# Kernel optimization log

Measured on AMD Instinct MI355X. Metric: run time of the kernel, lower is better.

The kernel has to match this reference:

```python
import jax, jax.numpy as jnp
import numpy as np

SIGMA = 2.0
EPS = 1e-8

N, P = 4, 64
Z, Y, X = 32, 128, 128


def setup_inputs() -> dict:
    key = jax.random.key(0)
    k1, k2 = jax.random.split(key)
    logits = jax.random.normal(k1, (N, 1, Z, Y, X), dtype=jnp.float32)
    # float (z,y,x) coordinates uniformly inside the grid
    dims = jnp.array([Z, Y, X], dtype=jnp.float32)
    pts = jax.random.uniform(k2, (N, P, 3), dtype=jnp.float32) * dims
    return {"logits": logits, "pts": pts}


def reference(logits, pts):
    # logits: [N,1,Z,Y,X]; pts: [N,P,3] in (z,y,x)
    n, _, z, y, x = logits.shape
    dt = logits.dtype
    s = jax.nn.sigmoid(logits[:, 0])  # [N,Z,Y,X]

    zz = jnp.arange(z, dtype=dt)
    yy = jnp.arange(y, dtype=dt)
    xx = jnp.arange(x, dtype=dt)

    # squared distances, broadcast to [N,P,Z,Y,X] only at the sum
    dz2 = (zz[None, None, :, None, None] - pts[:, :, 0, None, None, None]) ** 2  # [N,P,Z,1,1]
    dy2 = (yy[None, None, None, :, None] - pts[:, :, 1, None, None, None]) ** 2  # [N,P,1,Y,1]
    dx2 = (xx[None, None, None, None, :] - pts[:, :, 2, None, None, None]) ** 2  # [N,P,1,1,X]

    K = jnp.exp(-(dz2 + dy2 + dx2) / (2.0 * SIGMA * SIGMA))  # [N,P,Z,Y,X]
    denom = K.sum(axis=1)  # [N,Z,Y,X]  (alpha_bg == 0)
    w = s / jnp.maximum(denom, EPS)  # [N,Z,Y,X]
    # m_p = sum_v K[p,v] * s[v] / denom[v]
    m = jnp.einsum('npzyx,nzyx->np', K, w)  # [N,P]
    point_term = -jnp.log(jnp.maximum(m, EPS)).mean(axis=1)  # [N]
    return point_term.mean()  # reduction='mean'
```

## Files before the change

### kernel.cpp

```cpp
#include <hip/hip_runtime.h>
#include <math.h>

constexpr int N_ = 4, P_ = 64, Z_ = 32, Y_ = 128, X_ = 128;
constexpr float EPSF = 1e-8f;
constexpr float INV2S2 = 0.125f;

typedef short v8s __attribute__((ext_vector_type(8)));
typedef float v4f __attribute__((ext_vector_type(4)));

__device__ __forceinline__ short bf16(float f) {
    unsigned u = __float_as_uint(f);
    u = u + 0x7fffu + ((u >> 16) & 1u);
    return (short)(u >> 16);
}

__global__ __launch_bounds__(256) void k_main(const float* __restrict__ logits,
                                              const float* __restrict__ pts,
                                              float* __restrict__ part) {
    const int b = blockIdx.x;
    const int n  = b >> 6;
    const int z  = (b >> 1) & 31;
    const int y0 = (b & 1) * 64;

    const int tid  = threadIdx.x;
    const int lane = tid & 63;
    const int w    = tid >> 6;
    const int m    = lane & 15;
    const int quad = lane >> 4;

    __shared__ float ptsn[192];
    __shared__ short kxTB[128 * 64];
    __shared__ short WB[64 * 128];
    __shared__ float psum[64];

    if (tid < 192) ptsn[tid] = pts[n * 192 + tid];
    __syncthreads();

    for (int i = tid; i < 128 * 64; i += 256) {
        int x = i >> 6, p = i & 63;
        float dx = (float)x - ptsn[p * 3 + 2];
        float e = __expf(-dx * dx * INV2S2);
        kxTB[x * 64 + (((p >> 3) ^ (x & 7)) * 8) + (p & 7)] = bf16(e);
    }

    v8s a1[2];
    {
        float yv = (float)(y0 + w * 16 + m);
        #pragma unroll
        for (int ks = 0; ks < 2; ++ks) {
            #pragma unroll
            for (int j = 0; j < 8; ++j) {
                int p = ks * 32 + quad * 8 + j;
                float dz = (float)z - ptsn[p * 3 + 0];
                float dy = yv - ptsn[p * 3 + 1];
                a1[ks][j] = bf16(__expf(-(dz * dz + dy * dy) * INV2S2));
            }
        }
    }
    __syncthreads();

    v4f acc1[8];
    #pragma unroll
    for (int nt = 0; nt < 8; ++nt) acc1[nt] = (v4f)(0.f);
    #pragma unroll
    for (int ks = 0; ks < 2; ++ks) {
        #pragma unroll
        for (int nt = 0; nt < 8; ++nt) {
            int row = nt * 16 + m;
            int c = ks * 4 + quad;
            v8s bf = *(const v8s*)&kxTB[row * 64 + ((c ^ (row & 7)) * 8)];
            acc1[nt] = __builtin_amdgcn_mfma_f32_16x16x32_bf16(a1[ks], bf, acc1[nt], 0, 0, 0);
        }
    }

    {
        const float* lb = logits + (size_t)((n * Z_ + z) * Y_ + y0) * X_;
        float lgs[8][4];
        #pragma unroll
        for (int nt = 0; nt < 8; ++nt)
            #pragma unroll
            for (int reg = 0; reg < 4; ++reg)
                lgs[nt][reg] = lb[(w * 16 + quad * 4 + reg) * 128 + nt * 16 + m];
        #pragma unroll
        for (int nt = 0; nt < 8; ++nt) {
            #pragma unroll
            for (int reg = 0; reg < 4; ++reg) {
                int yl = w * 16 + quad * 4 + reg;
                int x  = nt * 16 + m;
                float wv = 1.0f / ((1.0f + __expf(-lgs[nt][reg])) *
                                   fmaxf(acc1[nt][reg], EPSF));
                WB[yl * 128 + (((x >> 3) ^ (yl & 15)) * 8) + (x & 7)] = bf16(wv);
            }
        }
    }

    v8s a2[4];
    {
        float px = ptsn[(w * 16 + m) * 3 + 2];
        #pragma unroll
        for (int ks = 0; ks < 4; ++ks) {
            #pragma unroll
            for (int j = 0; j < 8; ++j) {
                float dx = (float)(ks * 32 + quad * 8 + j) - px;
                a2[ks][j] = bf16(__expf(-dx * dx * INV2S2));
            }
        }
    }
    __syncthreads();

    v4f acc2[4];
    #pragma unroll
    for (int nt = 0; nt < 4; ++nt) acc2[nt] = (v4f)(0.f);
    #pragma unroll
    for (int ks = 0; ks < 4; ++ks) {
        #pragma unroll
        for (int nt = 0; nt < 4; ++nt) {
            int row = nt * 16 + m;
            int c = ks * 4 + quad;
            v8s bf = *(const v8s*)&WB[row * 128 + ((c ^ (row & 15)) * 8)];
            acc2[nt] = __builtin_amdgcn_mfma_f32_16x16x32_bf16(a2[ks], bf, acc2[nt], 0, 0, 0);
        }
    }

    float s[4] = {0.f, 0.f, 0.f, 0.f};
    #pragma unroll
    for (int reg = 0; reg < 4; ++reg) {
        int p = w * 16 + quad * 4 + reg;
        float pz = ptsn[p * 3 + 0], py = ptsn[p * 3 + 1];
        float dz = (float)z - pz;
        #pragma unroll
        for (int nt = 0; nt < 4; ++nt) {
            float dy = (float)(y0 + nt * 16 + m) - py;
            float kzy = __expf(-(dz * dz + dy * dy) * INV2S2);
            s[reg] = fmaf(acc2[nt][reg], kzy, s[reg]);
        }
    }
    #pragma unroll
    for (int reg = 0; reg < 4; ++reg)
        #pragma unroll
        for (int off = 1; off < 16; off <<= 1)
            s[reg] += __shfl_xor(s[reg], off, 64);
    if (m == 0) {
        #pragma unroll
        for (int reg = 0; reg < 4; ++reg)
            psum[w * 16 + quad * 4 + reg] = s[reg];
    }
    __syncthreads();
    if (tid < 64) part[b * 64 + tid] = psum[tid];
}

__global__ __launch_bounds__(1024) void k_finish(const float* __restrict__ part,
                                                 float* __restrict__ out) {
    const int t = threadIdx.x;
    const int pair = t & 255;
    const int quarter = t >> 8;
    const int n = pair >> 6, p = pair & 63;

    const float* base = part + (size_t)(n * 64 + quarter * 16) * 64 + p;
    float s0 = 0.f, s1 = 0.f, s2 = 0.f, s3 = 0.f;
    #pragma unroll
    for (int j = 0; j < 16; j += 4) {
        s0 += base[(j + 0) * 64];
        s1 += base[(j + 1) * 64];
        s2 += base[(j + 2) * 64];
        s3 += base[(j + 3) * 64];
    }
    __shared__ float red[4][256];
    red[quarter][pair] = (s0 + s1) + (s2 + s3);
    __syncthreads();

    if (t < 256) {
        const float mv = (red[0][t] + red[1][t]) + (red[2][t] + red[3][t]);
        float l = -logf(fmaxf(mv, EPSF));
        #pragma unroll
        for (int off = 32; off > 0; off >>= 1) l += __shfl_xor(l, off, 64);
        __shared__ float red2[4];
        if ((t & 63) == 0) red2[t >> 6] = l;
        __syncthreads();
        if (t == 0) out[0] = (red2[0] + red2[1] + red2[2] + red2[3]) * (1.0f / 256.0f);
    }
}

extern "C" void kernel_launch(void* const* d_in, const int* in_sizes, int n_in,
                              void* d_out, int out_size, void* d_ws, size_t ws_size,
                              hipStream_t stream) {
    const float* logits = (const float*)d_in[0];
    const float* pts    = (const float*)d_in[1];
    float* part = (float*)d_ws;
    float* out  = (float*)d_out;

    k_main<<<dim3(256), dim3(256), 0, stream>>>(logits, pts, part);
    k_finish<<<dim3(1), dim3(1024), 0, stream>>>(part, out);
}
```

Measured before the change: 66.53 us.

## Double k_main block to 512 threads and split MFMA tiles across eight waves

```diff
diff --git a/kernel.cpp b/kernel.cpp
--- a/kernel.cpp
+++ b/kernel.cpp
@@ -14,7 +14,7 @@
     return (short)(u >> 16);
 }
 
-__global__ __launch_bounds__(256) void k_main(const float* __restrict__ logits,
+__global__ __launch_bounds__(512) void k_main(const float* __restrict__ logits,
                                               const float* __restrict__ pts,
                                               float* __restrict__ part) {
     const int b = blockIdx.x;
@@ -27,16 +27,28 @@
     const int w    = tid >> 6;
     const int m    = lane & 15;
     const int quad = lane >> 4;
+    const int mt   = w & 3;
+    const int nh   = w >> 2;
+    const int pt   = w & 3;
+    const int yh   = w >> 2;
 
     __shared__ float ptsn[192];
     __shared__ short kxTB[128 * 64];
     __shared__ short WB[64 * 128];
-    __shared__ float psum[64];
+    __shared__ float psum[2][64];
+
+    const float* lb = logits + (size_t)((n * Z_ + z) * Y_ + y0) * X_;
+    float lgs[4][4];
+    #pragma unroll
+    for (int nt = 0; nt < 4; ++nt)
+        #pragma unroll
+        for (int reg = 0; reg < 4; ++reg)
+            lgs[nt][reg] = lb[(mt * 16 + quad * 4 + reg) * 128 + (nh * 4 + nt) * 16 + m];
 
     if (tid < 192) ptsn[tid] = pts[n * 192 + tid];
     __syncthreads();
 
-    for (int i = tid; i < 128 * 64; i += 256) {
+    for (int i = tid; i < 128 * 64; i += 512) {
         int x = i >> 6, p = i & 63;
         float dx = (float)x - ptsn[p * 3 + 2];
         float e = __expf(-dx * dx * INV2S2);
@@ -45,7 +57,7 @@
 
     v8s a1[2];
     {
-        float yv = (float)(y0 + w * 16 + m);
+        float yv = (float)(y0 + mt * 16 + m);
         #pragma unroll
         for (int ks = 0; ks < 2; ++ks) {
             #pragma unroll
@@ -59,44 +71,35 @@
     }
     __syncthreads();
 
-    v4f acc1[8];
+    v4f acc1[4];
     #pragma unroll
-    for (int nt = 0; nt < 8; ++nt) acc1[nt] = (v4f)(0.f);
+    for (int nt = 0; nt < 4; ++nt) acc1[nt] = (v4f)(0.f);
     #pragma unroll
     for (int ks = 0; ks < 2; ++ks) {
         #pragma unroll
-        for (int nt = 0; nt < 8; ++nt) {
-            int row = nt * 16 + m;
+        for (int nt = 0; nt < 4; ++nt) {
+            int row = (nh * 4 + nt) * 16 + m;
             int c = ks * 4 + quad;
             v8s bf = *(const v8s*)&kxTB[row * 64 + ((c ^ (row & 7)) * 8)];
             acc1[nt] = __builtin_amdgcn_mfma_f32_16x16x32_bf16(a1[ks], bf, acc1[nt], 0, 0, 0);
         }
     }
 
-    {
-        const float* lb = logits + (size_t)((n * Z_ + z) * Y_ + y0) * X_;
-        float lgs[8][4];
+    #pragma unroll
+    for (int nt = 0; nt < 4; ++nt) {
         #pragma unroll
-        for (int nt = 0; nt < 8; ++nt)
-            #pragma unroll
-            for (int reg = 0; reg < 4; ++reg)
-                lgs[nt][reg] = lb[(w * 16 + quad * 4 + reg) * 128 + nt * 16 + m];
-        #pragma unroll
-        for (int nt = 0; nt < 8; ++nt) {
-            #pragma unroll
-            for (int reg = 0; reg < 4; ++reg) {
-                int yl = w * 16 + quad * 4 + reg;
-                int x  = nt * 16 + m;
-                float wv = 1.0f / ((1.0f + __expf(-lgs[nt][reg])) *
-                                   fmaxf(acc1[nt][reg], EPSF));
-                WB[yl * 128 + (((x >> 3) ^ (yl & 15)) * 8) + (x & 7)] = bf16(wv);
-            }
+        for (int reg = 0; reg < 4; ++reg) {
+            int yl = mt * 16 + quad * 4 + reg;
+            int x  = (nh * 4 + nt) * 16 + m;
+            float wv = 1.0f / ((1.0f + __expf(-lgs[nt][reg])) *
+                               fmaxf(acc1[nt][reg], EPSF));
+            WB[yl * 128 + (((x >> 3) ^ (yl & 15)) * 8) + (x & 7)] = bf16(wv);
         }
     }
 
     v8s a2[4];
     {
-        float px = ptsn[(w * 16 + m) * 3 + 2];
+        float px = ptsn[(pt * 16 + m) * 3 + 2];
         #pragma unroll
         for (int ks = 0; ks < 4; ++ks) {
             #pragma unroll
@@ -108,14 +111,14 @@
     }
     __syncthreads();
 
-    v4f acc2[4];
-    #pragma unroll
-    for (int nt = 0; nt < 4; ++nt) acc2[nt] = (v4f)(0.f);
+    v4f acc2[2];
+    acc2[0] = (v4f)(0.f);
+    acc2[1] = (v4f)(0.f);
     #pragma unroll
     for (int ks = 0; ks < 4; ++ks) {
         #pragma unroll
-        for (int nt = 0; nt < 4; ++nt) {
-            int row = nt * 16 + m;
+        for (int nt = 0; nt < 2; ++nt) {
+            int row = (yh * 2 + nt) * 16 + m;
             int c = ks * 4 + quad;
             v8s bf = *(const v8s*)&WB[row * 128 + ((c ^ (row & 15)) * 8)];
             acc2[nt] = __builtin_amdgcn_mfma_f32_16x16x32_bf16(a2[ks], bf, acc2[nt], 0, 0, 0);
@@ -125,12 +128,12 @@
     float s[4] = {0.f, 0.f, 0.f, 0.f};
     #pragma unroll
     for (int reg = 0; reg < 4; ++reg) {
-        int p = w * 16 + quad * 4 + reg;
+        int p = pt * 16 + quad * 4 + reg;
         float pz = ptsn[p * 3 + 0], py = ptsn[p * 3 + 1];
         float dz = (float)z - pz;
         #pragma unroll
-        for (int nt = 0; nt < 4; ++nt) {
-            float dy = (float)(y0 + nt * 16 + m) - py;
+        for (int nt = 0; nt < 2; ++nt) {
+            float dy = (float)(y0 + (yh * 2 + nt) * 16 + m) - py;
             float kzy = __expf(-(dz * dz + dy * dy) * INV2S2);
             s[reg] = fmaf(acc2[nt][reg], kzy, s[reg]);
         }
@@ -143,10 +146,10 @@
     if (m == 0) {
         #pragma unroll
         for (int reg = 0; reg < 4; ++reg)
-            psum[w * 16 + quad * 4 + reg] = s[reg];
+            psum[yh][pt * 16 + quad * 4 + reg] = s[reg];
     }
     __syncthreads();
-    if (tid < 64) part[b * 64 + tid] = psum[tid];
+    if (tid < 64) part[b * 64 + tid] = psum[0][tid] + psum[1][tid];
 }
 
 __global__ __launch_bounds__(1024) void k_finish(const float* __restrict__ part,
@@ -189,6 +192,6 @@
     float* part = (float*)d_ws;
     float* out  = (float*)d_out;
 
-    k_main<<<dim3(256), dim3(256), 0, stream>>>(logits, pts, part);
+    k_main<<<dim3(256), dim3(512), 0, stream>>>(logits, pts, part);
     k_finish<<<dim3(1), dim3(1024), 0, stream>>>(part, out);
 }
```

After: 65.17 us (median of 2 runs). -2.0%, faster.
